# Kernel optimization log

Measured on AMD Instinct MI355X. Metric: run time of the kernel, lower is better.

## Reference

```python
import jax, jax.numpy as jnp
import numpy as np

D_MODEL = 1024
N_HEADS = 16
HEAD_DIM = D_MODEL // N_HEADS
ROPE_BASE = 10000.0


def setup_inputs() -> dict:
    key = jax.random.key(0)
    ks = jax.random.split(key, 5)
    B, S = 4, 2048
    bound_qkv = 1.0 / np.sqrt(D_MODEL)
    bound_out = 1.0 / np.sqrt(D_MODEL)
    return {
        "query": jax.random.normal(ks[0], (B, S, D_MODEL), dtype=jnp.float32),
        "W_qkv": jax.random.uniform(ks[1], (3 * D_MODEL, D_MODEL), jnp.float32, -bound_qkv, bound_qkv),
        "b_qkv": jax.random.uniform(ks[2], (3 * D_MODEL,), jnp.float32, -bound_qkv, bound_qkv),
        "W_out": jax.random.uniform(ks[3], (D_MODEL, D_MODEL), jnp.float32, -bound_out, bound_out),
        "b_out": jax.random.uniform(ks[4], (D_MODEL,), jnp.float32, -bound_out, bound_out),
    }


def _rope(x):
    # x: [B, H, S, Dh]; rotate-half RoPE, full rotational fraction
    S, Dh = x.shape[2], x.shape[3]
    half = Dh // 2
    inv_freq = 1.0 / (ROPE_BASE ** (jnp.arange(0, half, dtype=jnp.float32) * 2.0 / Dh))
    ang = jnp.arange(S, dtype=jnp.float32)[:, None] * inv_freq[None, :]  # [S, half]
    cos = jnp.concatenate([jnp.cos(ang), jnp.cos(ang)], axis=-1)  # [S, Dh]
    sin = jnp.concatenate([jnp.sin(ang), jnp.sin(ang)], axis=-1)
    x1, x2 = x[..., :half], x[..., half:]
    rot = jnp.concatenate([-x2, x1], axis=-1)
    return x * cos + rot * sin


def reference(query, W_qkv, b_qkv, W_out, b_out):
    B, S, _ = query.shape
    qkv = query @ W_qkv.T + b_qkv  # [B, S, 3*D]
    qkv = qkv.reshape(B, S, 3, N_HEADS, HEAD_DIM).transpose(2, 0, 3, 1, 4)  # [3, B, H, S, Dh]
    q, k, v = qkv[0], qkv[1], qkv[2]
    q = _rope(q)
    k = _rope(k)
    scale = 1.0 / np.sqrt(HEAD_DIM)
    scores = jnp.einsum("bhsd,bhtd->bhst", q, k) * scale  # [B, H, S, S]
    attn = jax.nn.softmax(scores, axis=-1)
    out = jnp.einsum("bhst,bhtd->bhsd", attn, v)  # [B, H, S, Dh]
    out = out.transpose(0, 2, 1, 3).reshape(B, S, D_MODEL)
    return out @ W_out.T + b_out
```

## Files before the change

### kernel.cpp

```cpp
#include <hip/hip_runtime.h>
#include <math.h>

#define D_MODEL 1024
#define N_HEADS 16
#define HEAD_DIM 64
#define BATCH 4
#define SEQ 2048
#define TOKENS (BATCH * SEQ)

typedef _Float16 f16;
typedef f16 f16x8_t __attribute__((ext_vector_type(8)));
typedef f16 f16x4_t __attribute__((ext_vector_type(4)));
typedef float f32x4_t __attribute__((ext_vector_type(4)));

#define QSCALE 0.18033688011112042f

__device__ __forceinline__ void stage16(const f16* g, f16* l) {
    __builtin_amdgcn_global_load_lds(
        (__attribute__((address_space(1))) void*)g,
        (__attribute__((address_space(3))) void*)l, 16, 0, 0);
}

__global__ void rope_table_kernel(float* __restrict__ cosT, float* __restrict__ sinT) {
    int idx = blockIdx.x * blockDim.x + threadIdx.x;
    int s = idx >> 5;
    int i = idx & 31;
    double t = (double)(2 * i) / 64.0;
    double invf = pow(10000.0, -t);
    double ang = (double)s * invf;
    cosT[idx] = (float)cos(ang);
    sinT[idx] = (float)sin(ang);
}

__global__ void convert_kernel(const float* __restrict__ in, f16* __restrict__ out,
                               int n4) {
    int i = blockIdx.x * blockDim.x + threadIdx.x;
    if (i >= n4) return;
    float4 x = ((const float4*)in)[i];
    f16x4_t h;
    h[0] = (f16)x.x; h[1] = (f16)x.y; h[2] = (f16)x.z; h[3] = (f16)x.w;
    ((f16x4_t*)out)[i] = h;
}

__device__ __forceinline__ void gemm_mainloop(
    const f16* __restrict__ A, const f16* __restrict__ B,
    int n0, int c0, f16* As, f16* Bs, f32x4_t acc[4][4]) {
    const int tid = threadIdx.x;
    const int lane = tid & 63;
    const int wave = tid >> 6;
    const int m16 = lane & 15, quad = lane >> 4;
    const int wm = (wave & 1) * 64, wn = (wave >> 1) * 64;

    const int srow = lane >> 3;
    const int scol = (lane & 7) << 3;

#pragma unroll
    for (int i = 0; i < 4; i++)
#pragma unroll
        for (int j = 0; j < 4; j++) acc[i][j] = (f32x4_t){0.f, 0.f, 0.f, 0.f};

    f16* ldsA = As + (wave * 32) * 64;
    f16* ldsB = Bs + (wave * 32) * 64;
    const f16* ga = A + (size_t)(n0 + wave * 32 + srow) * D_MODEL + scol;
    const f16* gb = B + (size_t)(c0 + wave * 32 + srow) * D_MODEL + scol;

    for (int kt = 0; kt < 16; kt++) {
        const int ko = kt * 64;
        __syncthreads();
#pragma unroll
        for (int inst = 0; inst < 4; inst++) {
            stage16(ga + ko + (size_t)(inst * 8) * D_MODEL, ldsA + inst * 8 * 64);
            stage16(gb + ko + (size_t)(inst * 8) * D_MODEL, ldsB + inst * 8 * 64);
        }
        __syncthreads();
#pragma unroll
        for (int kk = 0; kk < 2; kk++) {
            f16x8_t a[4], b[4];
#pragma unroll
            for (int mt = 0; mt < 4; mt++)
                a[mt] = *(const f16x8_t*)&As[(wm + mt * 16 + m16) * 64 + kk * 32 + quad * 8];
#pragma unroll
            for (int nt = 0; nt < 4; nt++)
                b[nt] = *(const f16x8_t*)&Bs[(wn + nt * 16 + m16) * 64 + kk * 32 + quad * 8];
#pragma unroll
            for (int mt = 0; mt < 4; mt++)
#pragma unroll
                for (int nt = 0; nt < 4; nt++)
                    acc[mt][nt] = __builtin_amdgcn_mfma_f32_16x16x32_f16(
                        a[mt], b[nt], acc[mt][nt], 0, 0, 0);
        }
    }
}

__global__ __launch_bounds__(256)
void qkv_gemm_kernel(const f16* __restrict__ Xf, const f16* __restrict__ Wf,
                     const float* __restrict__ bias,
                     f16* __restrict__ Qb, f16* __restrict__ Kb,
                     f16* __restrict__ VbT,
                     const float* __restrict__ cosT, const float* __restrict__ sinT) {
    __shared__ f16 As[128 * 64];
    __shared__ f16 Bs[128 * 64];
    f32x4_t acc[4][4];
    const int n0 = blockIdx.y * 128;
    const int c0 = blockIdx.x * 128;
    gemm_mainloop(Xf, Wf, n0, c0, As, Bs, acc);

    const int lane = threadIdx.x & 63;
    const int wave = threadIdx.x >> 6;
    const int m16 = lane & 15, quad = lane >> 4;
    const int wm = (wave & 1) * 64, wn = (wave >> 1) * 64;

    const int w = c0 >> 10;
    const int hh = ((c0 + wn) & 1023) >> 6;
    const int b = n0 >> 11;

    float bias4[4];
#pragma unroll
    for (int nt = 0; nt < 4; nt++) bias4[nt] = bias[c0 + wn + nt * 16 + m16];

    if (w == 2) {
        f16* vbase = VbT + ((size_t)(b * N_HEADS + hh) * HEAD_DIM) * SEQ;
#pragma unroll
        for (int mt = 0; mt < 4; mt++) {
            const int sb = (n0 + wm + mt * 16 + quad * 4) & (SEQ - 1);
#pragma unroll
            for (int nt = 0; nt < 4; nt++) {
                const int dh = nt * 16 + m16;
                f16x4_t v4;
#pragma unroll
                for (int i = 0; i < 4; i++) v4[i] = (f16)(acc[mt][nt][i] + bias4[nt]);
                *(f16x4_t*)&vbase[(size_t)dh * SEQ + sb] = v4;
            }
        }
        return;
    }

    f16* dst = (w == 0) ? Qb : Kb;
#pragma unroll
    for (int mt = 0; mt < 4; mt++)
#pragma unroll
        for (int i = 0; i < 4; i++) {
            const int n = n0 + wm + mt * 16 + quad * 4 + i;
            const int s = n & (SEQ - 1);
            f16* drow = dst + ((size_t)(b * N_HEADS + hh) * SEQ + s) * HEAD_DIM;
            float vv[4];
#pragma unroll
            for (int nt = 0; nt < 4; nt++) vv[nt] = acc[mt][nt][i] + bias4[nt];
            const float cs0 = cosT[(s << 5) + m16];
            const float sn0 = sinT[(s << 5) + m16];
            const float cs1 = cosT[(s << 5) + 16 + m16];
            const float sn1 = sinT[(s << 5) + 16 + m16];
#pragma unroll
            for (int nt = 0; nt < 4; nt++) {
                const int dh = nt * 16 + m16;
                const float cs = (nt & 1) ? cs1 : cs0;
                const float sn = (nt & 1) ? sn1 : sn0;
                const float part = vv[nt ^ 2];
                float outv = (nt >= 2) ? fmaf(vv[nt], cs, part * sn)
                                       : fmaf(vv[nt], cs, -part * sn);
                if (w == 0) outv *= QSCALE;
                drow[dh] = (f16)outv;
            }
        }
}

__global__ __launch_bounds__(256)
void out_gemm_kernel(const f16* __restrict__ Of, const f16* __restrict__ Wf,
                     const float* __restrict__ bias, float* __restrict__ Cout) {
    __shared__ f16 As[128 * 64];
    __shared__ f16 Bs[128 * 64];
    f32x4_t acc[4][4];
    const int n0 = blockIdx.y * 128;
    const int c0 = blockIdx.x * 128;
    gemm_mainloop(Of, Wf, n0, c0, As, Bs, acc);

    const int lane = threadIdx.x & 63;
    const int wave = threadIdx.x >> 6;
    const int m16 = lane & 15, quad = lane >> 4;
    const int wm = (wave & 1) * 64, wn = (wave >> 1) * 64;

    float bias4[4];
#pragma unroll
    for (int nt = 0; nt < 4; nt++) bias4[nt] = bias[c0 + wn + nt * 16 + m16];

#pragma unroll
    for (int mt = 0; mt < 4; mt++)
#pragma unroll
        for (int i = 0; i < 4; i++) {
            const int n = n0 + wm + mt * 16 + quad * 4 + i;
            float* orow = Cout + (size_t)n * D_MODEL + c0 + wn;
#pragma unroll
            for (int nt = 0; nt < 4; nt++)
                orow[nt * 16 + m16] = acc[mt][nt][i] + bias4[nt];
        }
}

#define KSW(row, g) ((g) ^ ((row) & 7))
__global__ __launch_bounds__(256, 4)
void attn_kernel(const f16* __restrict__ Qb, const f16* __restrict__ Kb,
                 const f16* __restrict__ VbT, f16* __restrict__ Of) {
    __shared__ f16 Ks[64 * 64];
    __shared__ f16 Vs[64 * 64];
    __shared__ f16 Ps[4][32][72];

    const int tid  = threadIdx.x;
    const int lane = tid & 63;
    const int wave = tid >> 6;
    const int m16  = lane & 15;
    const int quad = lane >> 4;

    const int bh = blockIdx.x >> 4;
    const int qt = blockIdx.x & 15;
    const int s0 = qt * 128;

    const f16* Kbase  = Kb + (size_t)bh * SEQ * HEAD_DIM;
    const f16* VtBase = VbT + (size_t)bh * HEAD_DIM * SEQ;

    f16x8_t bq[2][2];
#pragma unroll
    for (int nq = 0; nq < 2; nq++) {
        const f16* qrow = Qb + ((size_t)bh * SEQ + s0 + wave * 32 + nq * 16 + m16)
                          * HEAD_DIM + quad * 8;
        bq[nq][0] = *(const f16x8_t*)(qrow);
        bq[nq][1] = *(const f16x8_t*)(qrow + 32);
    }

    f32x4_t Oc[4][2];
#pragma unroll
    for (int mt = 0; mt < 4; mt++)
#pragma unroll
        for (int nq = 0; nq < 2; nq++) Oc[mt][nq] = (f32x4_t){0.f, 0.f, 0.f, 0.f};
    float sumacc[2] = {0.f, 0.f};

    const int lrow0 = wave * 16 + (lane >> 3);
    const int lrow1 = lrow0 + 8;
    const int gK0 = lrow0 * HEAD_DIM + KSW(lrow0, lane & 7) * 8;
    const int gK1 = lrow1 * HEAD_DIM + KSW(lrow1, lane & 7) * 8;
    const int gV0 = lrow0 * SEQ + KSW(lrow0, lane & 7) * 8;
    const int gV1 = lrow1 * SEQ + KSW(lrow1, lane & 7) * 8;
    f16* ldsK0 = Ks + (wave * 16) * 64;
    f16* ldsK1 = Ks + (wave * 16 + 8) * 64;
    f16* ldsV0 = Vs + (wave * 16) * 64;
    f16* ldsV1 = Vs + (wave * 16 + 8) * 64;

    for (int kt = 0; kt < SEQ / 64; kt++) {
        __syncthreads();
        const f16* kg = Kbase + (size_t)kt * 64 * HEAD_DIM;
        const f16* vg = VtBase + kt * 64;
        stage16(kg + gK0, ldsK0);
        stage16(kg + gK1, ldsK1);
        stage16(vg + gV0, ldsV0);
        stage16(vg + gV1, ldsV1);
        __syncthreads();

        f32x4_t Sc[4][2];
#pragma unroll
        for (int nt = 0; nt < 4; nt++)
#pragma unroll
            for (int nq = 0; nq < 2; nq++) Sc[nt][nq] = (f32x4_t){0.f, 0.f, 0.f, 0.f};
#pragma unroll
        for (int kki = 0; kki < 2; kki++) {
#pragma unroll
            for (int nt = 0; nt < 4; nt++) {
                const int row = nt * 16 + m16;
                f16x8_t ak = *(const f16x8_t*)&Ks[row * 64 + KSW(row, kki * 4 + quad) * 8];
#pragma unroll
                for (int nq = 0; nq < 2; nq++)
                    Sc[nt][nq] = __builtin_amdgcn_mfma_f32_16x16x32_f16(
                        ak, bq[nq][kki], Sc[nt][nq], 0, 0, 0);
            }
        }

#pragma unroll
        for (int nt = 0; nt < 4; nt++)
#pragma unroll
            for (int nq = 0; nq < 2; nq++) {
                f16x4_t pk4;
#pragma unroll
                for (int i = 0; i < 4; i++) {
                    float p = __builtin_amdgcn_exp2f(Sc[nt][nq][i]);
                    sumacc[nq] += p;
                    pk4[i] = (f16)p;
                }
                *(f16x4_t*)&Ps[wave][nq * 16 + m16][nt * 16 + quad * 4] = pk4;
            }

#pragma unroll
        for (int kki = 0; kki < 2; kki++) {
            f16x8_t bp[2];
#pragma unroll
            for (int nq = 0; nq < 2; nq++)
                bp[nq] = *(const f16x8_t*)&Ps[wave][nq * 16 + m16][kki * 32 + quad * 8];
#pragma unroll
            for (int mt = 0; mt < 4; mt++) {
                const int d = mt * 16 + m16;
                f16x8_t av = *(const f16x8_t*)&Vs[d * 64 + KSW(d, kki * 4 + quad) * 8];
#pragma unroll
                for (int nq = 0; nq < 2; nq++)
                    Oc[mt][nq] = __builtin_amdgcn_mfma_f32_16x16x32_f16(
                        av, bp[nq], Oc[mt][nq], 0, 0, 0);
            }
        }
    }

    const int b = bh >> 4, h = bh & 15;
#pragma unroll
    for (int nq = 0; nq < 2; nq++) {
        float l = sumacc[nq];
        l += __shfl_xor(l, 16);
        l += __shfl_xor(l, 32);
        const float invl = 1.0f / l;
        const int s = s0 + wave * 32 + nq * 16 + m16;
        const size_t off = ((size_t)(b * SEQ + s)) * D_MODEL + h * HEAD_DIM;
#pragma unroll
        for (int mt = 0; mt < 4; mt++) {
            f16x4_t o4;
#pragma unroll
            for (int i = 0; i < 4; i++)
                o4[i] = (f16)(Oc[mt][nq][i] * invl);
            *(f16x4_t*)&Of[off + mt * 16 + quad * 4] = o4;
        }
    }
}

extern "C" void kernel_launch(void* const* d_in, const int* in_sizes, int n_in,
                              void* d_out, int out_size, void* d_ws, size_t ws_size,
                              hipStream_t stream) {
    const float* X    = (const float*)d_in[0];
    const float* Wqkv = (const float*)d_in[1];
    const float* bqkv = (const float*)d_in[2];
    const float* Wout = (const float*)d_in[3];
    const float* bout = (const float*)d_in[4];
    float* out = (float*)d_out;

    char* w8 = (char*)d_ws;
    const size_t MB = 1024 * 1024;
    f16* Xf  = (f16*)(w8);
    f16* Wqf = (f16*)(w8 + 16 * MB);
    f16* Wof = (f16*)(w8 + 22 * MB);
    f16* Qf  = (f16*)(w8 + 24 * MB);
    f16* Kf  = (f16*)(w8 + 40 * MB);
    f16* VfT = (f16*)(w8 + 56 * MB);
    f16* Of  = (f16*)(w8 + 72 * MB);
    float* cosT = (float*)(w8 + 88 * MB);
    float* sinT = cosT + SEQ * 32;

    rope_table_kernel<<<(SEQ * 32) / 256, 256, 0, stream>>>(cosT, sinT);
    convert_kernel<<<(TOKENS * D_MODEL / 4) / 256, 256, 0, stream>>>(
        X, Xf, TOKENS * D_MODEL / 4);
    convert_kernel<<<(3 * D_MODEL * D_MODEL / 4) / 256, 256, 0, stream>>>(
        Wqkv, Wqf, 3 * D_MODEL * D_MODEL / 4);
    convert_kernel<<<(D_MODEL * D_MODEL / 4) / 256, 256, 0, stream>>>(
        Wout, Wof, D_MODEL * D_MODEL / 4);

    qkv_gemm_kernel<<<dim3(3 * D_MODEL / 128, TOKENS / 128), 256, 0, stream>>>(
        Xf, Wqf, bqkv, Qf, Kf, VfT, cosT, sinT);
    attn_kernel<<<BATCH * N_HEADS * (SEQ / 128), 256, 0, stream>>>(Qf, Kf, VfT, Of);
    out_gemm_kernel<<<dim3(D_MODEL / 128, TOKENS / 128), 256, 0, stream>>>(
        Of, Wof, bout, out);
}
```

Baseline: 298.4 us.

## Double attention query tile per block and merge fp16 conversion kernels

The attention kernel now gives each wave 64 query rows instead of 32, so every K/V tile staged into LDS feeds twice as many MFMAs. Block indexing is also reordered so consecutive blocks cover different heads, and launch bounds drop to 2 blocks per CU to leave room for the larger register tile. Separately, the three fp32-to-fp16 conversion launches are merged into one kernel to cut launch overhead. The costs are higher register pressure and half as many attention blocks (512), which lowers occupancy and latency hiding.

```diff
diff --git a/kernel.cpp b/kernel.cpp
--- a/kernel.cpp
+++ b/kernel.cpp
@@ -32,14 +32,25 @@
     sinT[idx] = (float)sin(ang);
 }
 
-__global__ void convert_kernel(const float* __restrict__ in, f16* __restrict__ out,
-                               int n4) {
+#define N_X  (TOKENS * D_MODEL / 4)
+#define N_WQ (3 * D_MODEL * D_MODEL / 4)
+#define N_WO (D_MODEL * D_MODEL / 4)
+__global__ void convert_all_kernel(const float* __restrict__ X,
+                                   const float* __restrict__ Wq,
+                                   const float* __restrict__ Wo,
+                                   f16* __restrict__ Xf, f16* __restrict__ Wqf,
+                                   f16* __restrict__ Wof) {
     int i = blockIdx.x * blockDim.x + threadIdx.x;
-    if (i >= n4) return;
-    float4 x = ((const float4*)in)[i];
+    const float* src;
+    f16* dst;
+    int j;
+    if (i < N_X)             { src = X;  dst = Xf;  j = i; }
+    else if (i < N_X + N_WQ) { src = Wq; dst = Wqf; j = i - N_X; }
+    else                     { src = Wo; dst = Wof; j = i - N_X - N_WQ; }
+    float4 x = ((const float4*)src)[j];
     f16x4_t h;
     h[0] = (f16)x.x; h[1] = (f16)x.y; h[2] = (f16)x.z; h[3] = (f16)x.w;
-    ((f16x4_t*)out)[i] = h;
+    ((f16x4_t*)dst)[j] = h;
 }
 
 __device__ __forceinline__ void gemm_mainloop(
@@ -196,12 +207,12 @@
 }
 
 #define KSW(row, g) ((g) ^ ((row) & 7))
-__global__ __launch_bounds__(256, 4)
+__global__ __launch_bounds__(256, 2)
 void attn_kernel(const f16* __restrict__ Qb, const f16* __restrict__ Kb,
                  const f16* __restrict__ VbT, f16* __restrict__ Of) {
     __shared__ f16 Ks[64 * 64];
     __shared__ f16 Vs[64 * 64];
-    __shared__ f16 Ps[4][32][72];
+    __shared__ f16 Ps[4][64][72];
 
     const int tid  = threadIdx.x;
     const int lane = tid & 63;
@@ -209,28 +220,28 @@
     const int m16  = lane & 15;
     const int quad = lane >> 4;
 
-    const int bh = blockIdx.x >> 4;
-    const int qt = blockIdx.x & 15;
-    const int s0 = qt * 128;
+    const int bh = blockIdx.x & 63;
+    const int qt = blockIdx.x >> 6;
+    const int s0 = qt * 256;
 
     const f16* Kbase  = Kb + (size_t)bh * SEQ * HEAD_DIM;
     const f16* VtBase = VbT + (size_t)bh * HEAD_DIM * SEQ;
 
-    f16x8_t bq[2][2];
-#pragma unroll
-    for (int nq = 0; nq < 2; nq++) {
-        const f16* qrow = Qb + ((size_t)bh * SEQ + s0 + wave * 32 + nq * 16 + m16)
+    f16x8_t bq[4][2];
+#pragma unroll
+    for (int nq = 0; nq < 4; nq++) {
+        const f16* qrow = Qb + ((size_t)bh * SEQ + s0 + wave * 64 + nq * 16 + m16)
                           * HEAD_DIM + quad * 8;
         bq[nq][0] = *(const f16x8_t*)(qrow);
         bq[nq][1] = *(const f16x8_t*)(qrow + 32);
     }
 
-    f32x4_t Oc[4][2];
+    f32x4_t Oc[4][4];
 #pragma unroll
     for (int mt = 0; mt < 4; mt++)
 #pragma unroll
-        for (int nq = 0; nq < 2; nq++) Oc[mt][nq] = (f32x4_t){0.f, 0.f, 0.f, 0.f};
-    float sumacc[2] = {0.f, 0.f};
+        for (int nq = 0; nq < 4; nq++) Oc[mt][nq] = (f32x4_t){0.f, 0.f, 0.f, 0.f};
+    float sumacc[4] = {0.f, 0.f, 0.f, 0.f};
 
     const int lrow0 = wave * 16 + (lane >> 3);
     const int lrow1 = lrow0 + 8;
@@ -253,11 +264,11 @@
         stage16(vg + gV1, ldsV1);
         __syncthreads();
 
-        f32x4_t Sc[4][2];
+        f32x4_t Sc[4][4];
 #pragma unroll
         for (int nt = 0; nt < 4; nt++)
 #pragma unroll
-            for (int nq = 0; nq < 2; nq++) Sc[nt][nq] = (f32x4_t){0.f, 0.f, 0.f, 0.f};
+            for (int nq = 0; nq < 4; nq++) Sc[nt][nq] = (f32x4_t){0.f, 0.f, 0.f, 0.f};
 #pragma unroll
         for (int kki = 0; kki < 2; kki++) {
 #pragma unroll
@@ -265,7 +276,7 @@
                 const int row = nt * 16 + m16;
                 f16x8_t ak = *(const f16x8_t*)&Ks[row * 64 + KSW(row, kki * 4 + quad) * 8];
 #pragma unroll
-                for (int nq = 0; nq < 2; nq++)
+                for (int nq = 0; nq < 4; nq++)
                     Sc[nt][nq] = __builtin_amdgcn_mfma_f32_16x16x32_f16(
                         ak, bq[nq][kki], Sc[nt][nq], 0, 0, 0);
             }
@@ -274,7 +285,7 @@
 #pragma unroll
         for (int nt = 0; nt < 4; nt++)
 #pragma unroll
-            for (int nq = 0; nq < 2; nq++) {
+            for (int nq = 0; nq < 4; nq++) {
                 f16x4_t pk4;
 #pragma unroll
                 for (int i = 0; i < 4; i++) {
@@ -287,16 +298,16 @@
 
 #pragma unroll
         for (int kki = 0; kki < 2; kki++) {
-            f16x8_t bp[2];
-#pragma unroll
-            for (int nq = 0; nq < 2; nq++)
+            f16x8_t bp[4];
+#pragma unroll
+            for (int nq = 0; nq < 4; nq++)
                 bp[nq] = *(const f16x8_t*)&Ps[wave][nq * 16 + m16][kki * 32 + quad * 8];
 #pragma unroll
             for (int mt = 0; mt < 4; mt++) {
                 const int d = mt * 16 + m16;
                 f16x8_t av = *(const f16x8_t*)&Vs[d * 64 + KSW(d, kki * 4 + quad) * 8];
 #pragma unroll
-                for (int nq = 0; nq < 2; nq++)
+                for (int nq = 0; nq < 4; nq++)
                     Oc[mt][nq] = __builtin_amdgcn_mfma_f32_16x16x32_f16(
                         av, bp[nq], Oc[mt][nq], 0, 0, 0);
             }
@@ -305,12 +316,12 @@
 
     const int b = bh >> 4, h = bh & 15;
 #pragma unroll
-    for (int nq = 0; nq < 2; nq++) {
+    for (int nq = 0; nq < 4; nq++) {
         float l = sumacc[nq];
         l += __shfl_xor(l, 16);
         l += __shfl_xor(l, 32);
         const float invl = 1.0f / l;
-        const int s = s0 + wave * 32 + nq * 16 + m16;
+        const int s = s0 + wave * 64 + nq * 16 + m16;
         const size_t off = ((size_t)(b * SEQ + s)) * D_MODEL + h * HEAD_DIM;
 #pragma unroll
         for (int mt = 0; mt < 4; mt++) {
@@ -346,16 +357,12 @@
     float* sinT = cosT + SEQ * 32;
 
     rope_table_kernel<<<(SEQ * 32) / 256, 256, 0, stream>>>(cosT, sinT);
-    convert_kernel<<<(TOKENS * D_MODEL / 4) / 256, 256, 0, stream>>>(
-        X, Xf, TOKENS * D_MODEL / 4);
-    convert_kernel<<<(3 * D_MODEL * D_MODEL / 4) / 256, 256, 0, stream>>>(
-        Wqkv, Wqf, 3 * D_MODEL * D_MODEL / 4);
-    convert_kernel<<<(D_MODEL * D_MODEL / 4) / 256, 256, 0, stream>>>(
-        Wout, Wof, D_MODEL * D_MODEL / 4);
+    convert_all_kernel<<<(N_X + N_WQ + N_WO) / 256, 256, 0, stream>>>(
+        X, Wqkv, Wout, Xf, Wqf, Wof);
 
     qkv_gemm_kernel<<<dim3(3 * D_MODEL / 128, TOKENS / 128), 256, 0, stream>>>(
         Xf, Wqf, bqkv, Qf, Kf, VfT, cosT, sinT);
-    attn_kernel<<<BATCH * N_HEADS * (SEQ / 128), 256, 0, stream>>>(Qf, Kf, VfT, Of);
+    attn_kernel<<<64 * (SEQ / 256), 256, 0, stream>>>(Qf, Kf, VfT, Of);
     out_gemm_kernel<<<dim3(D_MODEL / 128, TOKENS / 128), 256, 0, stream>>>(
         Of, Wof, bout, out);
 }
```

Measured after the change: 297.4 us. Within noise of the previous version (-0.3%).
